# Performance work log

Measured on AMD Instinct MI355X. Metric: run time of the kernel, lower is better.

## Reference

```python
import jax, jax.numpy as jnp
import numpy as np

GRAVITY = 9.81
W_INERTIA = 1.0
W_GRAVITY = 0.01
W_STRAIN = 1.0

V = 500_000
E = 2_000_000


def setup_inputs() -> dict:
    key = jax.random.key(0)
    ks = jax.random.split(key, 7)
    pos_next = jax.random.normal(ks[0], (V, 3), dtype=jnp.float32)
    pos_curr = jax.random.normal(ks[1], (V, 3), dtype=jnp.float32)
    pos_prev = jax.random.normal(ks[2], (V, 3), dtype=jnp.float32)
    mass = jax.random.uniform(ks[3], (V, 1), dtype=jnp.float32)
    elements = jax.random.randint(ks[4], (E, 4), 0, V, dtype=jnp.int64)
    rest_volumes = jax.random.uniform(ks[5], (E,), dtype=jnp.float32)
    rest_inv = jax.random.normal(ks[6], (E, 3, 3), dtype=jnp.float32)
    lam = jnp.float32(1.0)
    mu = jnpp_one = jnp.float32(1.0)
    return {
        "pos_next": pos_next, "pos_curr": pos_curr, "pos_prev": pos_prev,
        "mass": mass, "elements": elements, "rest_volumes": rest_volumes,
        "rest_inv": rest_inv, "lam": lam, "mu": mu,
    }


def _det3(F):
    # F: (E, 3, 3)
    return (F[:, 0, 0] * (F[:, 1, 1] * F[:, 2, 2] - F[:, 1, 2] * F[:, 2, 1])
            - F[:, 0, 1] * (F[:, 1, 0] * F[:, 2, 2] - F[:, 1, 2] * F[:, 2, 0])
            + F[:, 0, 2] * (F[:, 1, 0] * F[:, 2, 1] - F[:, 1, 1] * F[:, 2, 0]))


def _physics_loss(pos_next, pos_curr, pos_prev, mass, elements, rest_volumes, rest_inv, lam, mu):
    # Inertia: mean over all V*3 entries of 0.5 * m * a^2
    accel = pos_next + pos_prev - 2.0 * pos_curr          # (V, 3)
    inertia = 0.5 * jnp.mean(mass * accel * accel)
    # Gravity: -mean(m * g * y)
    gravity = -jnp.mean(mass * GRAVITY * pos_curr[:, 1:2])
    # Strain (Neo-Hookean) on pos_next
    v = pos_next[elements]                                 # (E, 4, 3)
    Ds = jnp.stack([v[:, 1] - v[:, 0], v[:, 2] - v[:, 0], v[:, 3] - v[:, 0]], axis=-1)  # (E,3,3)
    F_def = jnp.einsum('eij,ejk->eik', Ds, rest_inv)       # (E, 3, 3)
    det_F = jnp.maximum(_det3(F_def), 1e-8)
    log_det = jnp.log(det_F)
    tr_FtF = jnp.sum(F_def * F_def, axis=(1, 2))           # trace(F^T F) = ||F||_F^2
    psi = 0.5 * lam * log_det ** 2 - mu * log_det + 0.5 * mu * (tr_FtF - 3.0)
    strain = jnp.mean(psi * rest_volumes)
    return W_INERTIA * inertia + W_GRAVITY * gravity + W_STRAIN * strain


def reference(pos_next, pos_curr, pos_prev, mass, elements, rest_volumes, rest_inv, lam, mu):
    return _physics_loss(pos_next, pos_curr, pos_prev, mass, elements, rest_volumes, rest_inv, lam, mu)
```

## Files before the change

### kernel.cpp

```cpp
#include <hip/hip_runtime.h>

#define GRAVITY_F 9.81f

typedef int v4i __attribute__((ext_vector_type(4)));

__device__ __forceinline__ float blockReduceSum(float val) {
    #pragma unroll
    for (int off = 32; off > 0; off >>= 1)
        val += __shfl_down(val, off, 64);
    __shared__ float smem[16];
    const int lane = threadIdx.x & 63;
    const int wave = threadIdx.x >> 6;
    if (lane == 0) smem[wave] = val;
    __syncthreads();
    const int nwaves = (blockDim.x + 63) >> 6;
    val = 0.0f;
    if (wave == 0) {
        if (lane < nwaves) val = smem[lane];
        #pragma unroll
        for (int off = 8; off > 0; off >>= 1)
            val += __shfl_down(val, off, 64);
    }
    return val;
}

__device__ __forceinline__ float elem_term(const float* __restrict__ pn,
                                           const v4i idx,
                                           const float vol,
                                           const float* __restrict__ R,
                                           float lam, float mu, float sS) {
    float x0[3], x1[3], x2[3], x3[3];
    const float* v0 = pn + 3 * (size_t)idx.x;
    const float* v1 = pn + 3 * (size_t)idx.y;
    const float* v2 = pn + 3 * (size_t)idx.z;
    const float* v3 = pn + 3 * (size_t)idx.w;
    #pragma unroll
    for (int r = 0; r < 3; ++r) { x0[r] = v0[r]; x1[r] = v1[r]; x2[r] = v2[r]; x3[r] = v3[r]; }

    float Rv[9];
    #pragma unroll
    for (int k = 0; k < 9; ++k) Rv[k] = __builtin_nontemporal_load(R + k);

    float d[3][3];
    #pragma unroll
    for (int r = 0; r < 3; ++r) {
        d[r][0] = x1[r] - x0[r];
        d[r][1] = x2[r] - x0[r];
        d[r][2] = x3[r] - x0[r];
    }
    float F[3][3];
    #pragma unroll
    for (int r = 0; r < 3; ++r) {
        #pragma unroll
        for (int k = 0; k < 3; ++k)
            F[r][k] = d[r][0] * Rv[0 * 3 + k] + d[r][1] * Rv[1 * 3 + k] + d[r][2] * Rv[2 * 3 + k];
    }
    const float det = F[0][0] * (F[1][1] * F[2][2] - F[1][2] * F[2][1])
                    - F[0][1] * (F[1][0] * F[2][2] - F[1][2] * F[2][0])
                    + F[0][2] * (F[1][0] * F[2][1] - F[1][1] * F[2][0]);
    const float ld = logf(fmaxf(det, 1e-8f));
    float tr = 0.0f;
    #pragma unroll
    for (int r = 0; r < 3; ++r)
        #pragma unroll
        for (int k = 0; k < 3; ++k)
            tr += F[r][k] * F[r][k];
    const float psi = 0.5f * lam * ld * ld - mu * ld + 0.5f * mu * (tr - 3.0f);
    return sS * (psi * vol);
}

__global__ void fused_kernel(const float* __restrict__ pn,
                             const float* __restrict__ pc,
                             const float* __restrict__ pp,
                             const float* __restrict__ mass,
                             const int*   __restrict__ elems,
                             const float* __restrict__ vols,
                             const float* __restrict__ rinv,
                             const float* __restrict__ lam_p,
                             const float* __restrict__ mu_p,
                             float* __restrict__ partials,
                             int V, int E, int Vblocks,
                             float sI, float sG, float sS) {
    float local = 0.0f;

    if ((int)blockIdx.x < Vblocks) {
        const int v = blockIdx.x * blockDim.x + threadIdx.x;
        if (v < V) {
            const float m  = __builtin_nontemporal_load(mass + v);
            const float p0 = __builtin_nontemporal_load(pc + 3 * v + 0);
            const float y  = __builtin_nontemporal_load(pc + 3 * v + 1);
            const float p2 = __builtin_nontemporal_load(pc + 3 * v + 2);
            const float n0 = pn[3 * v + 0];
            const float n1 = pn[3 * v + 1];
            const float n2 = pn[3 * v + 2];
            const float q0 = __builtin_nontemporal_load(pp + 3 * v + 0);
            const float q1 = __builtin_nontemporal_load(pp + 3 * v + 1);
            const float q2 = __builtin_nontemporal_load(pp + 3 * v + 2);
            const float a0 = n0 + q0 - 2.0f * p0;
            const float a1 = n1 + q1 - 2.0f * y;
            const float a2 = n2 + q2 - 2.0f * p2;
            local = sI * (m * (a0 * a0 + a1 * a1 + a2 * a2)) + sG * (m * y);
        }
    } else {
        const float lam = lam_p[0];
        const float mu  = mu_p[0];
        const int base = (blockIdx.x - Vblocks) * (2 * blockDim.x);
        const int e0 = base + threadIdx.x;
        const int e1 = e0 + blockDim.x;

        v4i idx0 = (v4i)(0), idx1 = (v4i)(0);
        float vol0 = 0.0f, vol1 = 0.0f;
        const bool ok0 = e0 < E, ok1 = e1 < E;
        if (ok0) { idx0 = __builtin_nontemporal_load(((const v4i*)elems) + e0);
                   vol0 = __builtin_nontemporal_load(vols + e0); }
        if (ok1) { idx1 = __builtin_nontemporal_load(((const v4i*)elems) + e1);
                   vol1 = __builtin_nontemporal_load(vols + e1); }
        if (ok0) local += elem_term(pn, idx0, vol0, rinv + 9 * (size_t)e0, lam, mu, sS);
        if (ok1) local += elem_term(pn, idx1, vol1, rinv + 9 * (size_t)e1, lam, mu, sS);
    }

    const float tot = blockReduceSum(local);
    if (threadIdx.x == 0) partials[blockIdx.x] = tot;
}

__global__ void reduce_kernel(const float* __restrict__ partials, int n,
                              float* __restrict__ out) {
    double s = 0.0;
    for (int i = threadIdx.x; i < n; i += blockDim.x)
        s += (double)partials[i];
    __shared__ double sm[256];
    sm[threadIdx.x] = s;
    __syncthreads();
    #pragma unroll
    for (int off = 128; off > 0; off >>= 1) {
        if (threadIdx.x < off) sm[threadIdx.x] += sm[threadIdx.x + off];
        __syncthreads();
    }
    if (threadIdx.x == 0) out[0] = (float)sm[0];
}

extern "C" void kernel_launch(void* const* d_in, const int* in_sizes, int n_in,
                              void* d_out, int out_size, void* d_ws, size_t ws_size,
                              hipStream_t stream) {
    const float* pos_next = (const float*)d_in[0];
    const float* pos_curr = (const float*)d_in[1];
    const float* pos_prev = (const float*)d_in[2];
    const float* mass     = (const float*)d_in[3];
    const int*   elements = (const int*)d_in[4];
    const float* rest_vol = (const float*)d_in[5];
    const float* rest_inv = (const float*)d_in[6];
    const float* lam_p    = (const float*)d_in[7];
    const float* mu_p     = (const float*)d_in[8];
    float* out = (float*)d_out;

    const int V = in_sizes[3];
    const int E = in_sizes[5];

    const float sI = 0.5f / (3.0f * (float)V);
    const float sG = -0.01f * GRAVITY_F / (float)V;
    const float sS = 1.0f / (float)E;

    const int block = 256;
    const int Vblocks = (V + block - 1) / block;
    const int Eblocks = (E + 2 * block - 1) / (2 * block);
    const int grid = Vblocks + Eblocks;

    float* partials = (float*)d_ws;

    fused_kernel<<<grid, block, 0, stream>>>(pos_next, pos_curr, pos_prev,
                                             mass, elements, rest_vol,
                                             rest_inv, lam_p, mu_p,
                                             partials, V, E, Vblocks,
                                             sI, sG, sS);
    reduce_kernel<<<1, 256, 0, stream>>>(partials, grid, out);
}
```

Baseline: 226.7 us.

## Batch four elements per thread with hoisted loads and schedule element blocks first

```diff
diff --git a/kernel.cpp b/kernel.cpp
--- a/kernel.cpp
+++ b/kernel.cpp
@@ -24,67 +24,101 @@
     return val;
 }
 
-__device__ __forceinline__ float elem_term(const float* __restrict__ pn,
-                                           const v4i idx,
-                                           const float vol,
-                                           const float* __restrict__ R,
-                                           float lam, float mu, float sS) {
-    float x0[3], x1[3], x2[3], x3[3];
-    const float* v0 = pn + 3 * (size_t)idx.x;
-    const float* v1 = pn + 3 * (size_t)idx.y;
-    const float* v2 = pn + 3 * (size_t)idx.z;
-    const float* v3 = pn + 3 * (size_t)idx.w;
-    #pragma unroll
-    for (int r = 0; r < 3; ++r) { x0[r] = v0[r]; x1[r] = v1[r]; x2[r] = v2[r]; x3[r] = v3[r]; }
+#define EPT 4
 
-    float Rv[9];
-    #pragma unroll
-    for (int k = 0; k < 9; ++k) Rv[k] = __builtin_nontemporal_load(R + k);
-
-    float d[3][3];
-    #pragma unroll
-    for (int r = 0; r < 3; ++r) {
-        d[r][0] = x1[r] - x0[r];
-        d[r][1] = x2[r] - x0[r];
-        d[r][2] = x3[r] - x0[r];
-    }
-    float F[3][3];
-    #pragma unroll
-    for (int r = 0; r < 3; ++r) {
-        #pragma unroll
-        for (int k = 0; k < 3; ++k)
-            F[r][k] = d[r][0] * Rv[0 * 3 + k] + d[r][1] * Rv[1 * 3 + k] + d[r][2] * Rv[2 * 3 + k];
-    }
-    const float det = F[0][0] * (F[1][1] * F[2][2] - F[1][2] * F[2][1])
-                    - F[0][1] * (F[1][0] * F[2][2] - F[1][2] * F[2][0])
-                    + F[0][2] * (F[1][0] * F[2][1] - F[1][1] * F[2][0]);
-    const float ld = logf(fmaxf(det, 1e-8f));
-    float tr = 0.0f;
-    #pragma unroll
-    for (int r = 0; r < 3; ++r)
-        #pragma unroll
-        for (int k = 0; k < 3; ++k)
-            tr += F[r][k] * F[r][k];
-    const float psi = 0.5f * lam * ld * ld - mu * ld + 0.5f * mu * (tr - 3.0f);
-    return sS * (psi * vol);
-}
-
-__global__ void fused_kernel(const float* __restrict__ pn,
-                             const float* __restrict__ pc,
-                             const float* __restrict__ pp,
-                             const float* __restrict__ mass,
-                             const int*   __restrict__ elems,
-                             const float* __restrict__ vols,
-                             const float* __restrict__ rinv,
-                             const float* __restrict__ lam_p,
-                             const float* __restrict__ mu_p,
-                             float* __restrict__ partials,
-                             int V, int E, int Vblocks,
-                             float sI, float sG, float sS) {
+__global__ void __launch_bounds__(256, 4)
+fused_kernel(const float* __restrict__ pn,
+             const float* __restrict__ pc,
+             const float* __restrict__ pp,
+             const float* __restrict__ mass,
+             const int*   __restrict__ elems,
+             const float* __restrict__ vols,
+             const float* __restrict__ rinv,
+             const float* __restrict__ lam_p,
+             const float* __restrict__ mu_p,
+             float* __restrict__ partials,
+             int V, int E, int Eblocks,
+             float sI, float sG, float sS) {
     float local = 0.0f;
 
-    if ((int)blockIdx.x < Vblocks) {
-        const int v = blockIdx.x * blockDim.x + threadIdx.x;
+    if ((int)blockIdx.x < Eblocks) {
+        const float lam = lam_p[0];
+        const float mu  = mu_p[0];
+        const int base = blockIdx.x * (EPT * 256) + threadIdx.x;
+
+        int  ec[EPT];
+        float sc[EPT];
+        #pragma unroll
+        for (int i = 0; i < EPT; ++i) {
+            const int e = base + i * 256;
+            ec[i] = e < E ? e : (E - 1);
+            sc[i] = e < E ? sS : 0.0f;
+        }
+        v4i  idx[EPT];
+        float vol[EPT];
+        #pragma unroll
+        for (int i = 0; i < EPT; ++i) {
+            idx[i] = __builtin_nontemporal_load(((const v4i*)elems) + ec[i]);
+            vol[i] = __builtin_nontemporal_load(vols + ec[i]);
+        }
+
+        float x[EPT][4][3];
+        #pragma unroll
+        for (int i = 0; i < EPT; ++i) {
+            const float* v0 = pn + 3 * (size_t)idx[i].x;
+            const float* v1 = pn + 3 * (size_t)idx[i].y;
+            const float* v2 = pn + 3 * (size_t)idx[i].z;
+            const float* v3 = pn + 3 * (size_t)idx[i].w;
+            #pragma unroll
+            for (int r = 0; r < 3; ++r) {
+                x[i][0][r] = v0[r];
+                x[i][1][r] = v1[r];
+                x[i][2][r] = v2[r];
+                x[i][3][r] = v3[r];
+            }
+        }
+
+        float R[EPT][9];
+        #pragma unroll
+        for (int i = 0; i < EPT; ++i) {
+            const float* Rp = rinv + 9 * (size_t)ec[i];
+            #pragma unroll
+            for (int k = 0; k < 9; ++k)
+                R[i][k] = __builtin_nontemporal_load(Rp + k);
+        }
+
+        #pragma unroll
+        for (int i = 0; i < EPT; ++i) {
+            float d[3][3];
+            #pragma unroll
+            for (int r = 0; r < 3; ++r) {
+                d[r][0] = x[i][1][r] - x[i][0][r];
+                d[r][1] = x[i][2][r] - x[i][0][r];
+                d[r][2] = x[i][3][r] - x[i][0][r];
+            }
+            float F[3][3];
+            #pragma unroll
+            for (int r = 0; r < 3; ++r)
+                #pragma unroll
+                for (int k = 0; k < 3; ++k)
+                    F[r][k] = d[r][0] * R[i][0 * 3 + k]
+                            + d[r][1] * R[i][1 * 3 + k]
+                            + d[r][2] * R[i][2 * 3 + k];
+            const float det = F[0][0] * (F[1][1] * F[2][2] - F[1][2] * F[2][1])
+                            - F[0][1] * (F[1][0] * F[2][2] - F[1][2] * F[2][0])
+                            + F[0][2] * (F[1][0] * F[2][1] - F[1][1] * F[2][0]);
+            const float ld = logf(fmaxf(det, 1e-8f));
+            float tr = 0.0f;
+            #pragma unroll
+            for (int r = 0; r < 3; ++r)
+                #pragma unroll
+                for (int k = 0; k < 3; ++k)
+                    tr += F[r][k] * F[r][k];
+            const float psi = 0.5f * lam * ld * ld - mu * ld + 0.5f * mu * (tr - 3.0f);
+            local += sc[i] * (psi * vol[i]);
+        }
+    } else {
+        const int v = (blockIdx.x - Eblocks) * blockDim.x + threadIdx.x;
         if (v < V) {
             const float m  = __builtin_nontemporal_load(mass + v);
             const float p0 = __builtin_nontemporal_load(pc + 3 * v + 0);
@@ -101,22 +135,6 @@
             const float a2 = n2 + q2 - 2.0f * p2;
             local = sI * (m * (a0 * a0 + a1 * a1 + a2 * a2)) + sG * (m * y);
         }
-    } else {
-        const float lam = lam_p[0];
-        const float mu  = mu_p[0];
-        const int base = (blockIdx.x - Vblocks) * (2 * blockDim.x);
-        const int e0 = base + threadIdx.x;
-        const int e1 = e0 + blockDim.x;
-
-        v4i idx0 = (v4i)(0), idx1 = (v4i)(0);
-        float vol0 = 0.0f, vol1 = 0.0f;
-        const bool ok0 = e0 < E, ok1 = e1 < E;
-        if (ok0) { idx0 = __builtin_nontemporal_load(((const v4i*)elems) + e0);
-                   vol0 = __builtin_nontemporal_load(vols + e0); }
-        if (ok1) { idx1 = __builtin_nontemporal_load(((const v4i*)elems) + e1);
-                   vol1 = __builtin_nontemporal_load(vols + e1); }
-        if (ok0) local += elem_term(pn, idx0, vol0, rinv + 9 * (size_t)e0, lam, mu, sS);
-        if (ok1) local += elem_term(pn, idx1, vol1, rinv + 9 * (size_t)e1, lam, mu, sS);
     }
 
     const float tot = blockReduceSum(local);
@@ -161,16 +179,16 @@
     const float sS = 1.0f / (float)E;
 
     const int block = 256;
+    const int Eblocks = (E + EPT * block - 1) / (EPT * block);
     const int Vblocks = (V + block - 1) / block;
-    const int Eblocks = (E + 2 * block - 1) / (2 * block);
-    const int grid = Vblocks + Eblocks;
+    const int grid = Eblocks + Vblocks;
 
     float* partials = (float*)d_ws;
 
     fused_kernel<<<grid, block, 0, stream>>>(pos_next, pos_curr, pos_prev,
                                              mass, elements, rest_vol,
                                              rest_inv, lam_p, mu_p,
-                                             partials, V, E, Vblocks,
+                                             partials, V, E, Eblocks,
                                              sI, sG, sS);
     reduce_kernel<<<1, 256, 0, stream>>>(partials, grid, out);
 }
```

New measurement: 223.2 us. Within noise of the previous version (-1.5%).
